# Performance work log

Measured on AMD Instinct MI355X. Metric: run time of the kernel, lower is better.

## Reference

```python
import jax, jax.numpy as jnp
import numpy as np

B, S, H, F, E, K = 2, 2048, 1024, 2816, 8, 2

def setup_inputs() -> dict:
    key = jax.random.key(0)
    k0, k1, k2, k3, k4 = jax.random.split(key, 5)
    return {
        "hidden_states": jax.random.normal(k0, (B, S, H), dtype=jnp.float32),
        "router_w": jax.random.normal(k1, (E, H), dtype=jnp.float32) * (1.0 / np.sqrt(H)),
        "w_gate": jax.random.normal(k2, (E, H, F), dtype=jnp.float32) * (1.0 / np.sqrt(H)),
        "w_up": jax.random.normal(k3, (E, H, F), dtype=jnp.float32) * (1.0 / np.sqrt(H)),
        "w_down": jax.random.normal(k4, (E, F, H), dtype=jnp.float32) * (1.0 / np.sqrt(F)),
    }

def reference(hidden_states, router_w, w_gate, w_up, w_down):
    # Router: logits [B,S,E], top-k routing with softmax over the k selected logits.
    router_logits = jnp.einsum("bsh,eh->bse", hidden_states, router_w)
    topk_values, topk_indices = jax.lax.top_k(router_logits, K)  # [B,S,K]
    topk_weights = jax.nn.softmax(topk_values.astype(jnp.float32), axis=-1).astype(hidden_states.dtype)

    x = hidden_states.reshape(-1, H)            # [T,H], T = B*S
    flat_idx = topk_indices.reshape(-1, K)      # [T,K] (int)
    flat_w = topk_weights.reshape(-1, K)        # [T,K]

    mixed = jnp.zeros_like(x)
    for e in range(E):  # small fixed expert loop; tokens fully vectorized
        # per-token combine weight for expert e (0 if not routed here)
        w_e = jnp.sum(jnp.where(flat_idx == e, flat_w, jnp.zeros_like(flat_w)), axis=-1)[:, None]
        # SwiGLU expert MLP: down(silu(gate(x)) * up(x))
        y = (jax.nn.silu(x @ w_gate[e]) * (x @ w_up[e])) @ w_down[e]
        mixed = mixed + w_e * y
    mixed_output = mixed.reshape(hidden_states.shape)

    # Load-balancing aux loss (Switch-style)
    router_probs = jax.nn.softmax(router_logits.astype(jnp.float32), axis=-1)
    P = router_probs.mean(axis=(0, 1))                                   # [E]
    f = jax.nn.one_hot(topk_indices, E, dtype=jnp.float32).mean(axis=(0, 1, 2))  # [E]
    aux_loss = E * jnp.sum(f * P)
    return mixed_output, aux_loss
```

## Files before the change

### kernel.cpp

```cpp
#include <hip/hip_runtime.h>
#include <hip/hip_bf16.h>
#include <stdint.h>

#define T_TOK 4096
#define H_DIM 1024
#define F_DIM 2816
#define E_NUM 8
#define ROWS_CAP 9216
#define TOTAL_MT 72

typedef float  f32x4  __attribute__((ext_vector_type(4)));
typedef __bf16 bf16x8 __attribute__((ext_vector_type(8)));

__device__ __forceinline__ unsigned short f32_bf16(float f) {
  union { float f; unsigned u; } v; v.f = f;
  unsigned r = v.u + 0x7fffu + ((v.u >> 16) & 1u);
  return (unsigned short)(r >> 16);
}

__device__ __forceinline__ void async16(const void* g, void* l) {
  __builtin_amdgcn_global_load_lds(
      (__attribute__((address_space(1))) void*)(g),
      (__attribute__((address_space(3))) void*)(l),
      16, 0, 0);
}

__device__ __forceinline__ f32x4 mfma16(bf16x8 a, bf16x8 b, f32x4 c) {
  return __builtin_amdgcn_mfma_f32_16x16x32_bf16(a, b, c, 0, 0, 0);
}


__global__ __launch_bounds__(256) void conv_x_kernel(const float* __restrict__ x,
                                                     unsigned short* __restrict__ xb) {
  int i = blockIdx.x * 256 + threadIdx.x;
  float4 v = ((const float4*)x)[i];
  ushort4 o;
  o.x = f32_bf16(v.x); o.y = f32_bf16(v.y); o.z = f32_bf16(v.z); o.w = f32_bf16(v.w);
  ((ushort4*)xb)[i] = o;
}

__global__ __launch_bounds__(256) void transpose_all(const float* __restrict__ wg,
                                                     const float* __restrict__ wu,
                                                     const float* __restrict__ wd,
                                                     unsigned short* __restrict__ Wgt,
                                                     unsigned short* __restrict__ Wut,
                                                     unsigned short* __restrict__ Wdt) {
  int mz = blockIdx.z >> 3, e = blockIdx.z & 7;
  const float* s; unsigned short* d; int R, C;
  size_t mat = (size_t)H_DIM * F_DIM;
  if (mz == 0)      { s = wg + e * mat; d = Wgt + e * mat; R = H_DIM; C = F_DIM; }
  else if (mz == 1) { s = wu + e * mat; d = Wut + e * mat; R = H_DIM; C = F_DIM; }
  else              { s = wd + e * mat; d = Wdt + e * mat; R = F_DIM; C = H_DIM; }
  int c0 = blockIdx.x * 64, r0 = blockIdx.y * 64;
  if (c0 >= C || r0 >= R) return;

  __shared__ float tile[64 * 65];
  int tid = threadIdx.x;
  int rr = tid >> 4, c4 = tid & 15;
#pragma unroll
  for (int it = 0; it < 4; it++) {
    int r = rr + 16 * it;
    float4 v = *(const float4*)(s + (size_t)(r0 + r) * C + c0 + c4 * 4);
    tile[r * 65 + c4 * 4 + 0] = v.x;
    tile[r * 65 + c4 * 4 + 1] = v.y;
    tile[r * 65 + c4 * 4 + 2] = v.z;
    tile[r * 65 + c4 * 4 + 3] = v.w;
  }
  __syncthreads();
  int cc = tid >> 4, r4 = tid & 15;
#pragma unroll
  for (int it = 0; it < 4; it++) {
    int c = cc + 16 * it;
    ushort4 o;
    o.x = f32_bf16(tile[(r4 * 4 + 0) * 65 + c]);
    o.y = f32_bf16(tile[(r4 * 4 + 1) * 65 + c]);
    o.z = f32_bf16(tile[(r4 * 4 + 2) * 65 + c]);
    o.w = f32_bf16(tile[(r4 * 4 + 3) * 65 + c]);
    *(ushort4*)(d + (size_t)(c0 + c) * R + r0 + r4 * 4) = o;
  }
}


__global__ __launch_bounds__(256) void router_kernel(const float* __restrict__ x,
                                                     const float* __restrict__ rw,
                                                     int* __restrict__ t2i,
                                                     float* __restrict__ t2w,
                                                     int* __restrict__ counts,
                                                     float* __restrict__ psum) {
  __shared__ float srw[E_NUM * H_DIM];
  __shared__ float sP[E_NUM];
  __shared__ int sC[E_NUM];
  int tid = threadIdx.x;
  for (int i = tid; i < E_NUM * H_DIM; i += 256) srw[i] = rw[i];
  if (tid < E_NUM) { sP[tid] = 0.f; sC[tid] = 0; }
  __syncthreads();
  int w = tid >> 6, lane = tid & 63;
  for (int it = 0; it < 4; ++it) {
    int t = blockIdx.x * 16 + w * 4 + it;
    float acc[E_NUM];
#pragma unroll
    for (int e = 0; e < E_NUM; e++) acc[e] = 0.f;
    const float* xr = x + (size_t)t * H_DIM;
    for (int h = lane; h < H_DIM; h += 64) {
      float xv = xr[h];
#pragma unroll
      for (int e = 0; e < E_NUM; e++) acc[e] += xv * srw[e * H_DIM + h];
    }
#pragma unroll
    for (int e = 0; e < E_NUM; e++) {
      float v = acc[e];
      for (int o = 32; o > 0; o >>= 1) v += __shfl_down(v, o, 64);
      acc[e] = __shfl(v, 0, 64);
    }
    if (lane == 0) {
      float mx = acc[0];
#pragma unroll
      for (int e = 1; e < E_NUM; e++) mx = fmaxf(mx, acc[e]);
      float pr[E_NUM], s = 0.f;
#pragma unroll
      for (int e = 0; e < E_NUM; e++) { pr[e] = __expf(acc[e] - mx); s += pr[e]; }
      float inv = 1.f / s;
#pragma unroll
      for (int e = 0; e < E_NUM; e++) atomicAdd(&sP[e], pr[e] * inv);
      int i0 = 0; float v0 = acc[0];
#pragma unroll
      for (int e = 1; e < E_NUM; e++) if (acc[e] > v0) { v0 = acc[e]; i0 = e; }
      int i1 = -1; float v1 = -3.4e38f;
#pragma unroll
      for (int e = 0; e < E_NUM; e++) if (e != i0 && acc[e] > v1) { v1 = acc[e]; i1 = e; }
      float e1 = __expf(v1 - v0);
      float w0 = 1.f / (1.f + e1);
      t2i[2 * t] = i0; t2i[2 * t + 1] = i1;
      t2w[2 * t] = w0; t2w[2 * t + 1] = e1 * w0;
      atomicAdd(&sC[i0], 1); atomicAdd(&sC[i1], 1);
    }
  }
  __syncthreads();
  if (tid < E_NUM) { atomicAdd(&counts[tid], sC[tid]); atomicAdd(&psum[tid], sP[tid]); }
}

__global__ void scan_aux_kernel(const int* __restrict__ counts, const float* __restrict__ psum,
                                int* __restrict__ offsets, int* __restrict__ cursors,
                                float* __restrict__ aux_out) {
  if (threadIdx.x == 0 && blockIdx.x == 0) {
    int off = 0; float aux = 0.f;
    for (int e = 0; e < E_NUM; e++) {
      offsets[e] = off;
      cursors[e] = off;
      off += (counts[e] + 127) & ~127;
      aux += ((float)counts[e] / 8192.0f) * (psum[e] / 4096.0f);
    }
    offsets[E_NUM] = off;
    *aux_out = 8.0f * aux;
  }
}

__global__ __launch_bounds__(256) void assign_kernel(const int* __restrict__ t2i,
                                                     const float* __restrict__ t2w,
                                                     int* __restrict__ cursors,
                                                     int* __restrict__ row2token,
                                                     float* __restrict__ roww,
                                                     int* __restrict__ t2row) {
  int t = blockIdx.x * 256 + threadIdx.x;
#pragma unroll
  for (int s = 0; s < 2; s++) {
    int e = t2i[2 * t + s];
    int p = atomicAdd(&cursors[e], 1);
    row2token[p] = t;
    roww[p] = t2w[2 * t + s];
    t2row[2 * t + s] = p;
  }
}

__device__ __forceinline__ int find_expert(const int* __restrict__ offsets, int row0,
                                           int& off_out) {
  int esel = -1, off = 0;
#pragma unroll
  for (int e = 0; e < E_NUM; e++) {
    int lo = offsets[e], hi = offsets[e + 1];
    if (row0 >= lo && row0 < hi) { esel = e; off = lo; }
  }
  off_out = off;
  return esel;
}

__global__ __launch_bounds__(256) void gateup_kernel(
    const unsigned short* __restrict__ xb,
    const unsigned short* __restrict__ wgt,
    const unsigned short* __restrict__ wut,
    unsigned short* __restrict__ act,
    const int* __restrict__ counts, const int* __restrict__ offsets,
    const int* __restrict__ row2token) {
  int g = blockIdx.x;
  int row0 = g * 128;
  int off;
  int e = find_expert(offsets, row0, off);
  if (e < 0) return;
  int cnt = counts[e];
  int rowbase = row0 - off;
  int ntile = blockIdx.y;

  __shared__ __align__(16) unsigned short smA[128 * 32];
  __shared__ __align__(16) unsigned short smG[128 * 32];
  __shared__ __align__(16) unsigned short smU[128 * 32];

  int tid = threadIdx.x;
  int w = tid >> 6, lane = tid & 63;
  int wm = w & 1, wn = w >> 1;

  int r0 = tid >> 2, q0 = tid & 3;
  int r1 = r0 + 64;
  int tok0 = (rowbase + r0 < cnt) ? row2token[off + rowbase + r0] : 0;
  int tok1 = (rowbase + r1 < cnt) ? row2token[off + rowbase + r1] : 0;
  const unsigned short* gA0 = xb + (size_t)tok0 * H_DIM + q0 * 8;
  const unsigned short* gA1 = xb + (size_t)tok1 * H_DIM + q0 * 8;
  size_t wb = (size_t)e * F_DIM * H_DIM;
  const unsigned short* gG0 = wgt + wb + (size_t)(ntile * 128 + r0) * H_DIM + q0 * 8;
  const unsigned short* gG1 = wgt + wb + (size_t)(ntile * 128 + r1) * H_DIM + q0 * 8;
  const unsigned short* gU0 = wut + wb + (size_t)(ntile * 128 + r0) * H_DIM + q0 * 8;
  const unsigned short* gU1 = wut + wb + (size_t)(ntile * 128 + r1) * H_DIM + q0 * 8;
  unsigned short* lA0 = smA + tid * 8;
  unsigned short* lA1 = smA + (tid + 256) * 8;
  unsigned short* lG0 = smG + tid * 8;
  unsigned short* lG1 = smG + (tid + 256) * 8;
  unsigned short* lU0 = smU + tid * 8;
  unsigned short* lU1 = smU + (tid + 256) * 8;

  f32x4 accg[4][4], accu[4][4];
#pragma unroll
  for (int i = 0; i < 4; i++)
#pragma unroll
    for (int j = 0; j < 4; j++) {
      accg[i][j] = (f32x4){0.f, 0.f, 0.f, 0.f};
      accu[i][j] = (f32x4){0.f, 0.f, 0.f, 0.f};
    }

  int m = lane & 15, quad = lane >> 4;
  for (int k0 = 0; k0 < H_DIM; k0 += 32) {
    async16(gA0 + k0, lA0);
    async16(gA1 + k0, lA1);
    async16(gG0 + k0, lG0);
    async16(gG1 + k0, lG1);
    async16(gU0 + k0, lU0);
    async16(gU1 + k0, lU1);
    __syncthreads();
    bf16x8 a[4], bg[4], bu[4];
#pragma unroll
    for (int i = 0; i < 4; i++)
      a[i] = *(const bf16x8*)(smA + (wm * 64 + 16 * i + m) * 32 + quad * 8);
#pragma unroll
    for (int j = 0; j < 4; j++) {
      bg[j] = *(const bf16x8*)(smG + (wn * 64 + 16 * j + m) * 32 + quad * 8);
      bu[j] = *(const bf16x8*)(smU + (wn * 64 + 16 * j + m) * 32 + quad * 8);
    }
#pragma unroll
    for (int i = 0; i < 4; i++)
#pragma unroll
      for (int j = 0; j < 4; j++) {
        accg[i][j] = mfma16(a[i], bg[j], accg[i][j]);
        accu[i][j] = mfma16(a[i], bu[j], accu[i][j]);
      }
    __syncthreads();
  }

#pragma unroll
  for (int i = 0; i < 4; i++)
#pragma unroll
    for (int j = 0; j < 4; j++)
#pragma unroll
      for (int r = 0; r < 4; r++) {
        int rt = wm * 64 + 16 * i + quad * 4 + r;
        int ct = wn * 64 + 16 * j + m;
        float g2 = accg[i][j][r], u = accu[i][j][r];
        float sv = g2 / (1.f + __expf(-g2)) * u;
        act[(size_t)(off + rowbase + rt) * F_DIM + ntile * 128 + ct] = f32_bf16(sv);
      }
}

__global__ __launch_bounds__(256) void down_kernel(
    const unsigned short* __restrict__ act,
    const unsigned short* __restrict__ wdt,
    const int* __restrict__ counts, const int* __restrict__ offsets,
    const float* __restrict__ roww,
    float* __restrict__ Y) {
  int g = blockIdx.x;
  int row0 = g * 128;
  int off;
  int e = find_expert(offsets, row0, off);
  if (e < 0) return;
  int cnt = counts[e];
  int rowbase = row0 - off;
  int ntile = blockIdx.y;

  __shared__ __align__(16) unsigned short smA[128 * 32];
  __shared__ __align__(16) unsigned short smB[128 * 32];

  int tid = threadIdx.x;
  int w = tid >> 6, lane = tid & 63;
  int wm = w & 1, wn = w >> 1;

  int r0 = tid >> 2, q0 = tid & 3;
  int r1 = r0 + 64;
  const unsigned short* gA0 = act + (size_t)(off + rowbase + r0) * F_DIM + q0 * 8;
  const unsigned short* gA1 = act + (size_t)(off + rowbase + r1) * F_DIM + q0 * 8;
  size_t wb = (size_t)e * H_DIM * F_DIM;
  const unsigned short* gB0 = wdt + wb + (size_t)(ntile * 128 + r0) * F_DIM + q0 * 8;
  const unsigned short* gB1 = wdt + wb + (size_t)(ntile * 128 + r1) * F_DIM + q0 * 8;
  unsigned short* lA0 = smA + tid * 8;
  unsigned short* lA1 = smA + (tid + 256) * 8;
  unsigned short* lB0 = smB + tid * 8;
  unsigned short* lB1 = smB + (tid + 256) * 8;

  f32x4 acc[4][4];
#pragma unroll
  for (int i = 0; i < 4; i++)
#pragma unroll
    for (int j = 0; j < 4; j++) acc[i][j] = (f32x4){0.f, 0.f, 0.f, 0.f};

  int m = lane & 15, quad = lane >> 4;
  for (int k0 = 0; k0 < F_DIM; k0 += 32) {
    async16(gA0 + k0, lA0);
    async16(gA1 + k0, lA1);
    async16(gB0 + k0, lB0);
    async16(gB1 + k0, lB1);
    __syncthreads();
    bf16x8 a[4], b[4];
#pragma unroll
    for (int i = 0; i < 4; i++) {
      a[i] = *(const bf16x8*)(smA + (wm * 64 + 16 * i + m) * 32 + quad * 8);
      b[i] = *(const bf16x8*)(smB + (wn * 64 + 16 * i + m) * 32 + quad * 8);
    }
#pragma unroll
    for (int i = 0; i < 4; i++)
#pragma unroll
      for (int j = 0; j < 4; j++) acc[i][j] = mfma16(a[i], b[j], acc[i][j]);
    __syncthreads();
  }

#pragma unroll
  for (int i = 0; i < 4; i++)
#pragma unroll
    for (int r = 0; r < 4; r++) {
      int rt = wm * 64 + 16 * i + quad * 4 + r;
      int lrow = rowbase + rt;
      if (lrow < cnt) {
        float cw = roww[off + lrow];
#pragma unroll
        for (int j = 0; j < 4; j++) {
          int h = ntile * 128 + wn * 64 + 16 * j + m;
          Y[(size_t)(off + lrow) * H_DIM + h] = cw * acc[i][j][r];
        }
      }
    }
}

__global__ __launch_bounds__(256) void combine_kernel(const float* __restrict__ Y,
                                                      const int* __restrict__ t2row,
                                                      float* __restrict__ out) {
  int t = blockIdx.x, hc = threadIdx.x;
  int r0 = t2row[2 * t], r1 = t2row[2 * t + 1];
  float4 a = ((const float4*)(Y + (size_t)r0 * H_DIM))[hc];
  float4 b = ((const float4*)(Y + (size_t)r1 * H_DIM))[hc];
  float4 o; o.x = a.x + b.x; o.y = a.y + b.y; o.z = a.z + b.z; o.w = a.w + b.w;
  ((float4*)(out + (size_t)t * H_DIM))[hc] = o;
}


extern "C" void kernel_launch(void* const* d_in, const int* in_sizes, int n_in,
                              void* d_out, int out_size, void* d_ws, size_t ws_size,
                              hipStream_t stream) {
  const float* x  = (const float*)d_in[0];
  const float* rw = (const float*)d_in[1];
  const float* wg = (const float*)d_in[2];
  const float* wu = (const float*)d_in[3];
  const float* wd = (const float*)d_in[4];
  float* out = (float*)d_out;

  char* ws = (char*)d_ws;
  size_t p = 0;
  auto alloc = [&](size_t bytes) {
    char* r = ws + p;
    p = (p + bytes + 255) & ~(size_t)255;
    return r;
  };
  unsigned short* Xb  = (unsigned short*)alloc((size_t)T_TOK * H_DIM * 2);
  unsigned short* Wgt = (unsigned short*)alloc((size_t)E_NUM * F_DIM * H_DIM * 2);
  unsigned short* Wut = (unsigned short*)alloc((size_t)E_NUM * F_DIM * H_DIM * 2);
  unsigned short* Wdt = (unsigned short*)alloc((size_t)E_NUM * H_DIM * F_DIM * 2);
  unsigned short* Act = (unsigned short*)alloc((size_t)ROWS_CAP * F_DIM * 2);
  int*   t2i = (int*)alloc(T_TOK * 2 * 4);
  float* t2w = (float*)alloc(T_TOK * 2 * 4);
  int*   t2row = (int*)alloc(T_TOK * 2 * 4);
  int*   row2token = (int*)alloc(ROWS_CAP * 4);
  float* roww = (float*)alloc(ROWS_CAP * 4);
  int* ctrs = (int*)alloc(64 * 4);
  int* counts  = ctrs;
  int* cursors = ctrs + 8;
  float* psum  = (float*)(ctrs + 16);
  int* offsets = ctrs + 24;
  float* Y = (float*)Wgt;

  hipMemsetAsync(ctrs, 0, 96, stream);

  conv_x_kernel<<<T_TOK * H_DIM / 4 / 256, 256, 0, stream>>>(x, Xb);
  transpose_all<<<dim3(F_DIM / 64, F_DIM / 64, 24), 256, 0, stream>>>(wg, wu, wd, Wgt, Wut, Wdt);

  router_kernel<<<T_TOK / 16, 256, 0, stream>>>(x, rw, t2i, t2w, counts, psum);
  scan_aux_kernel<<<1, 64, 0, stream>>>(counts, psum, offsets, cursors, out + (size_t)T_TOK * H_DIM);
  assign_kernel<<<T_TOK / 256, 256, 0, stream>>>(t2i, t2w, cursors, row2token, roww, t2row);

  gateup_kernel<<<dim3(TOTAL_MT, F_DIM / 128), 256, 0, stream>>>(Xb, Wgt, Wut, Act, counts, offsets, row2token);
  down_kernel<<<dim3(TOTAL_MT, H_DIM / 128), 256, 0, stream>>>(Act, Wdt, counts, offsets, roww, Y);
  combine_kernel<<<T_TOK, 256, 0, stream>>>(Y, t2row, out);
}
```

Measured before the change: 708.1 us.

## Split down GEMM over K, narrow gate/up N tile, compact transpose grid

The down-projection is split into two K halves via a third grid dimension. Each half writes its own partial Y buffer, and the combine kernel sums the four partials per token. The gate/up kernel drops its N tile from 128 to 64 columns, doubling block count and cutting accumulator registers. The weight transpose launch is remapped to a dense 1D-per-expert grid so it no longer launches many blocks that exit immediately. The goal is more parallelism and occupancy. The cost is twice the Y write traffic plus extra reads in combine, and less A-tile reuse in gate/up.

```diff
diff --git a/kernel.cpp b/kernel.cpp
--- a/kernel.cpp
+++ b/kernel.cpp
@@ -45,14 +45,18 @@
                                                      unsigned short* __restrict__ Wgt,
                                                      unsigned short* __restrict__ Wut,
                                                      unsigned short* __restrict__ Wdt) {
-  int mz = blockIdx.z >> 3, e = blockIdx.z & 7;
-  const float* s; unsigned short* d; int R, C;
+  int bx = blockIdx.x;
+  int mz = bx / 704, local = bx % 704;
+  const float* s; unsigned short* d; int R, C, tx;
   size_t mat = (size_t)H_DIM * F_DIM;
-  if (mz == 0)      { s = wg + e * mat; d = Wgt + e * mat; R = H_DIM; C = F_DIM; }
-  else if (mz == 1) { s = wu + e * mat; d = Wut + e * mat; R = H_DIM; C = F_DIM; }
-  else              { s = wd + e * mat; d = Wdt + e * mat; R = F_DIM; C = H_DIM; }
-  int c0 = blockIdx.x * 64, r0 = blockIdx.y * 64;
-  if (c0 >= C || r0 >= R) return;
+  if (mz == 0)      { s = wg; d = Wgt; R = H_DIM; C = F_DIM; tx = 44; }
+  else if (mz == 1) { s = wu; d = Wut; R = H_DIM; C = F_DIM; tx = 44; }
+  else              { s = wd; d = Wdt; R = F_DIM; C = H_DIM; tx = 16; }
+  int c0 = (local % tx) * 64;
+  int rg0 = (local / tx) * 64;
+  int e = blockIdx.y;
+  s += e * mat; d += e * mat;
+  int r0 = rg0;
 
   __shared__ float tile[64 * 65];
   int tid = threadIdx.x;
@@ -201,36 +205,33 @@
   int ntile = blockIdx.y;
 
   __shared__ __align__(16) unsigned short smA[128 * 32];
-  __shared__ __align__(16) unsigned short smG[128 * 32];
-  __shared__ __align__(16) unsigned short smU[128 * 32];
+  __shared__ __align__(16) unsigned short smG[64 * 32];
+  __shared__ __align__(16) unsigned short smU[64 * 32];
 
   int tid = threadIdx.x;
   int w = tid >> 6, lane = tid & 63;
   int wm = w & 1, wn = w >> 1;
 
-  int r0 = tid >> 2, q0 = tid & 3;
-  int r1 = r0 + 64;
-  int tok0 = (rowbase + r0 < cnt) ? row2token[off + rowbase + r0] : 0;
-  int tok1 = (rowbase + r1 < cnt) ? row2token[off + rowbase + r1] : 0;
-  const unsigned short* gA0 = xb + (size_t)tok0 * H_DIM + q0 * 8;
-  const unsigned short* gA1 = xb + (size_t)tok1 * H_DIM + q0 * 8;
+  int cA0 = w * 64 + lane;
+  int rA0 = cA0 >> 2, qA0 = cA0 & 3;
+  int rA1 = rA0 + 64;
+  int tok0 = (rowbase + rA0 < cnt) ? row2token[off + rowbase + rA0] : 0;
+  int tok1 = (rowbase + rA1 < cnt) ? row2token[off + rowbase + rA1] : 0;
+  const unsigned short* gA0 = xb + (size_t)tok0 * H_DIM + qA0 * 8;
+  const unsigned short* gA1 = xb + (size_t)tok1 * H_DIM + qA0 * 8;
   size_t wb = (size_t)e * F_DIM * H_DIM;
-  const unsigned short* gG0 = wgt + wb + (size_t)(ntile * 128 + r0) * H_DIM + q0 * 8;
-  const unsigned short* gG1 = wgt + wb + (size_t)(ntile * 128 + r1) * H_DIM + q0 * 8;
-  const unsigned short* gU0 = wut + wb + (size_t)(ntile * 128 + r0) * H_DIM + q0 * 8;
-  const unsigned short* gU1 = wut + wb + (size_t)(ntile * 128 + r1) * H_DIM + q0 * 8;
-  unsigned short* lA0 = smA + tid * 8;
-  unsigned short* lA1 = smA + (tid + 256) * 8;
-  unsigned short* lG0 = smG + tid * 8;
-  unsigned short* lG1 = smG + (tid + 256) * 8;
-  unsigned short* lU0 = smU + tid * 8;
-  unsigned short* lU1 = smU + (tid + 256) * 8;
-
-  f32x4 accg[4][4], accu[4][4];
+  const unsigned short* gG = wgt + wb + (size_t)(ntile * 64 + rA0) * H_DIM + qA0 * 8;
+  const unsigned short* gU = wut + wb + (size_t)(ntile * 64 + rA0) * H_DIM + qA0 * 8;
+  unsigned short* lA0 = smA + (w * 64) * 8;
+  unsigned short* lA1 = smA + (256 + w * 64) * 8;
+  unsigned short* lG = smG + (w * 64) * 8;
+  unsigned short* lU = smU + (w * 64) * 8;
+
+  f32x4 accg[4][2], accu[4][2];
 #pragma unroll
   for (int i = 0; i < 4; i++)
 #pragma unroll
-    for (int j = 0; j < 4; j++) {
+    for (int j = 0; j < 2; j++) {
       accg[i][j] = (f32x4){0.f, 0.f, 0.f, 0.f};
       accu[i][j] = (f32x4){0.f, 0.f, 0.f, 0.f};
     }
@@ -239,24 +240,22 @@
   for (int k0 = 0; k0 < H_DIM; k0 += 32) {
     async16(gA0 + k0, lA0);
     async16(gA1 + k0, lA1);
-    async16(gG0 + k0, lG0);
-    async16(gG1 + k0, lG1);
-    async16(gU0 + k0, lU0);
-    async16(gU1 + k0, lU1);
+    async16(gG + k0, lG);
+    async16(gU + k0, lU);
     __syncthreads();
-    bf16x8 a[4], bg[4], bu[4];
+    bf16x8 a[4], bg[2], bu[2];
 #pragma unroll
     for (int i = 0; i < 4; i++)
       a[i] = *(const bf16x8*)(smA + (wm * 64 + 16 * i + m) * 32 + quad * 8);
 #pragma unroll
-    for (int j = 0; j < 4; j++) {
-      bg[j] = *(const bf16x8*)(smG + (wn * 64 + 16 * j + m) * 32 + quad * 8);
-      bu[j] = *(const bf16x8*)(smU + (wn * 64 + 16 * j + m) * 32 + quad * 8);
+    for (int j = 0; j < 2; j++) {
+      bg[j] = *(const bf16x8*)(smG + (wn * 32 + 16 * j + m) * 32 + quad * 8);
+      bu[j] = *(const bf16x8*)(smU + (wn * 32 + 16 * j + m) * 32 + quad * 8);
     }
 #pragma unroll
     for (int i = 0; i < 4; i++)
 #pragma unroll
-      for (int j = 0; j < 4; j++) {
+      for (int j = 0; j < 2; j++) {
         accg[i][j] = mfma16(a[i], bg[j], accg[i][j]);
         accu[i][j] = mfma16(a[i], bu[j], accu[i][j]);
       }
@@ -266,14 +265,14 @@
 #pragma unroll
   for (int i = 0; i < 4; i++)
 #pragma unroll
-    for (int j = 0; j < 4; j++)
+    for (int j = 0; j < 2; j++)
 #pragma unroll
       for (int r = 0; r < 4; r++) {
         int rt = wm * 64 + 16 * i + quad * 4 + r;
-        int ct = wn * 64 + 16 * j + m;
+        int ct = wn * 32 + 16 * j + m;
         float g2 = accg[i][j][r], u = accu[i][j][r];
         float sv = g2 / (1.f + __expf(-g2)) * u;
-        act[(size_t)(off + rowbase + rt) * F_DIM + ntile * 128 + ct] = f32_bf16(sv);
+        act[(size_t)(off + rowbase + rt) * F_DIM + ntile * 64 + ct] = f32_bf16(sv);
       }
 }
 
@@ -291,6 +290,8 @@
   int cnt = counts[e];
   int rowbase = row0 - off;
   int ntile = blockIdx.y;
+  int ks = blockIdx.z;
+  int kbase = ks * (F_DIM / 2);
 
   __shared__ __align__(16) unsigned short smA[128 * 32];
   __shared__ __align__(16) unsigned short smB[128 * 32];
@@ -301,11 +302,11 @@
 
   int r0 = tid >> 2, q0 = tid & 3;
   int r1 = r0 + 64;
-  const unsigned short* gA0 = act + (size_t)(off + rowbase + r0) * F_DIM + q0 * 8;
-  const unsigned short* gA1 = act + (size_t)(off + rowbase + r1) * F_DIM + q0 * 8;
+  const unsigned short* gA0 = act + (size_t)(off + rowbase + r0) * F_DIM + kbase + q0 * 8;
+  const unsigned short* gA1 = act + (size_t)(off + rowbase + r1) * F_DIM + kbase + q0 * 8;
   size_t wb = (size_t)e * H_DIM * F_DIM;
-  const unsigned short* gB0 = wdt + wb + (size_t)(ntile * 128 + r0) * F_DIM + q0 * 8;
-  const unsigned short* gB1 = wdt + wb + (size_t)(ntile * 128 + r1) * F_DIM + q0 * 8;
+  const unsigned short* gB0 = wdt + wb + (size_t)(ntile * 128 + r0) * F_DIM + kbase + q0 * 8;
+  const unsigned short* gB1 = wdt + wb + (size_t)(ntile * 128 + r1) * F_DIM + kbase + q0 * 8;
   unsigned short* lA0 = smA + tid * 8;
   unsigned short* lA1 = smA + (tid + 256) * 8;
   unsigned short* lB0 = smB + tid * 8;
@@ -318,7 +319,7 @@
     for (int j = 0; j < 4; j++) acc[i][j] = (f32x4){0.f, 0.f, 0.f, 0.f};
 
   int m = lane & 15, quad = lane >> 4;
-  for (int k0 = 0; k0 < F_DIM; k0 += 32) {
+  for (int k0 = 0; k0 < F_DIM / 2; k0 += 32) {
     async16(gA0 + k0, lA0);
     async16(gA1 + k0, lA1);
     async16(gB0 + k0, lB0);
@@ -337,6 +338,7 @@
     __syncthreads();
   }
 
+  float* Yk = Y + (size_t)ks * ROWS_CAP * H_DIM;
 #pragma unroll
   for (int i = 0; i < 4; i++)
 #pragma unroll
@@ -348,7 +350,7 @@
 #pragma unroll
         for (int j = 0; j < 4; j++) {
           int h = ntile * 128 + wn * 64 + 16 * j + m;
-          Y[(size_t)(off + lrow) * H_DIM + h] = cw * acc[i][j][r];
+          Yk[(size_t)(off + lrow) * H_DIM + h] = cw * acc[i][j][r];
         }
       }
     }
@@ -359,9 +361,16 @@
                                                       float* __restrict__ out) {
   int t = blockIdx.x, hc = threadIdx.x;
   int r0 = t2row[2 * t], r1 = t2row[2 * t + 1];
-  float4 a = ((const float4*)(Y + (size_t)r0 * H_DIM))[hc];
-  float4 b = ((const float4*)(Y + (size_t)r1 * H_DIM))[hc];
-  float4 o; o.x = a.x + b.x; o.y = a.y + b.y; o.z = a.z + b.z; o.w = a.w + b.w;
+  const float* Y1 = Y + (size_t)ROWS_CAP * H_DIM;
+  float4 a = ((const float4*)(Y  + (size_t)r0 * H_DIM))[hc];
+  float4 b = ((const float4*)(Y  + (size_t)r1 * H_DIM))[hc];
+  float4 c = ((const float4*)(Y1 + (size_t)r0 * H_DIM))[hc];
+  float4 d = ((const float4*)(Y1 + (size_t)r1 * H_DIM))[hc];
+  float4 o;
+  o.x = (a.x + b.x) + (c.x + d.x);
+  o.y = (a.y + b.y) + (c.y + d.y);
+  o.z = (a.z + b.z) + (c.z + d.z);
+  o.w = (a.w + b.w) + (c.w + d.w);
   ((float4*)(out + (size_t)t * H_DIM))[hc] = o;
 }
 
@@ -403,13 +412,13 @@
   hipMemsetAsync(ctrs, 0, 96, stream);
 
   conv_x_kernel<<<T_TOK * H_DIM / 4 / 256, 256, 0, stream>>>(x, Xb);
-  transpose_all<<<dim3(F_DIM / 64, F_DIM / 64, 24), 256, 0, stream>>>(wg, wu, wd, Wgt, Wut, Wdt);
+  transpose_all<<<dim3(2112, E_NUM), 256, 0, stream>>>(wg, wu, wd, Wgt, Wut, Wdt);
 
   router_kernel<<<T_TOK / 16, 256, 0, stream>>>(x, rw, t2i, t2w, counts, psum);
   scan_aux_kernel<<<1, 64, 0, stream>>>(counts, psum, offsets, cursors, out + (size_t)T_TOK * H_DIM);
   assign_kernel<<<T_TOK / 256, 256, 0, stream>>>(t2i, t2w, cursors, row2token, roww, t2row);
 
-  gateup_kernel<<<dim3(TOTAL_MT, F_DIM / 128), 256, 0, stream>>>(Xb, Wgt, Wut, Act, counts, offsets, row2token);
-  down_kernel<<<dim3(TOTAL_MT, H_DIM / 128), 256, 0, stream>>>(Act, Wdt, counts, offsets, roww, Y);
+  gateup_kernel<<<dim3(TOTAL_MT, F_DIM / 64), 256, 0, stream>>>(Xb, Wgt, Wut, Act, counts, offsets, row2token);
+  down_kernel<<<dim3(TOTAL_MT, H_DIM / 128, 2), 256, 0, stream>>>(Act, Wdt, counts, offsets, roww, Y);
   combine_kernel<<<T_TOK, 256, 0, stream>>>(Y, t2row, out);
 }
```

Measured after the change: 626.2 us. 1.13x faster.
